# Optimization experiments

Measured on AMD Instinct MI355X. Metric: run time of the kernel, lower is better.

Reference implementation:

```python
import jax, jax.numpy as jnp
from jax import lax
import numpy as np

B, C, H, W = 4, 1024, 64, 64
HEAD_DIM = 8
HEADS = C // HEAD_DIM  # 128
EPS = 1e-15
BN_EPS = 1e-5
DN = ('NCHW', 'OIHW', 'NCHW')


def setup_inputs() -> dict:
    key = jax.random.key(0)
    ks = jax.random.split(key, 8)
    s = lambda k, shp, scale: jax.random.normal(k, shp, jnp.float32) * scale
    return {
        'x': s(ks[0], (B, C, H, W), 1.0),
        'Wq': s(ks[1], (C, C), C ** -0.5),
        'Wk': s(ks[2], (C, C), C ** -0.5),
        'Wv': s(ks[3], (C, C), C ** -0.5),
        'dw_w': s(ks[4], (3 * C, 1, 5, 5), 0.2),          # depthwise, groups=3C
        'pw_w': s(ks[5], (3 * C, HEAD_DIM, 1, 1), 0.3),   # 1x1 grouped, groups=3*heads
        'Wout': s(ks[6], (C, 2 * C), (2 * C) ** -0.5),
        'gamma': jnp.ones((C,), jnp.float32),
        'beta': jnp.zeros((C,), jnp.float32),
    }


def _forward(x, Wq, Wk, Wv, dw_w, pw_w, Wout, gamma, beta):
    b, c, h, w = x.shape
    n = h * w
    hbhwc = jnp.moveaxis(x, 1, -1)                      # B H W C
    q = hbhwc @ Wq.T
    k = hbhwc @ Wk.T
    v = hbhwc @ Wv.T
    qkv = jnp.moveaxis(jnp.concatenate([q, k, v], -1), -1, 1)  # B 3C H W
    # multiscale branch: depthwise kxk then grouped 1x1
    ms = lax.conv_general_dilated(qkv, dw_w, (1, 1), 'SAME',
                                  feature_group_count=3 * c, dimension_numbers=DN)
    ms = lax.conv_general_dilated(ms, pw_w, (1, 1), 'VALID',
                                  feature_group_count=3 * HEADS, dimension_numbers=DN)
    hs = jnp.concatenate([qkv, ms], axis=1)             # B 6C H W
    hs = hs.astype(jnp.float32).reshape(b, -1, 3 * HEAD_DIM, n)  # B ht 3d N
    q, k, v = jnp.split(hs, 3, axis=2)                  # each B ht d N
    q = jax.nn.relu(q)
    k = jax.nn.relu(k)
    v = jnp.pad(v, ((0, 0), (0, 0), (0, 1), (0, 0)), constant_values=1.0)  # B ht d+1 N
    scores = jnp.einsum('bhdn,bhen->bhde', v, k)        # B ht d+1 d
    out = jnp.einsum('bhde,bhen->bhdn', scores, q)      # B ht d+1 N
    out = out[:, :, :-1] / (out[:, :, -1:] + EPS)       # B ht d N
    out = out.reshape(b, -1, h, w)                      # B 2C H W
    out = jnp.moveaxis(jnp.moveaxis(out, 1, -1) @ Wout.T, -1, 1)  # B C H W
    # batch norm (batch statistics, affine)
    mean = out.mean(axis=(0, 2, 3), keepdims=True)
    var = out.var(axis=(0, 2, 3), keepdims=True)
    gb = lambda p: p[None, :, None, None]
    return (out - mean) * lax.rsqrt(var + BN_EPS) * gb(gamma) + gb(beta)


def reference(x, Wq, Wk, Wv, dw_w, pw_w, Wout, gamma, beta):
    return _forward(x, Wq, Wk, Wv, dw_w, pw_w, Wout, gamma, beta)
```

## Files before the change

kernel.cpp:

```cpp
#include <hip/hip_runtime.h>


typedef short bf16x8 __attribute__((ext_vector_type(8)));
typedef float f32x4 __attribute__((ext_vector_type(4)));

__device__ __forceinline__ float bf2f(unsigned short u) {
  union { unsigned int i; float f; } w; w.i = ((unsigned int)u) << 16; return w.f;
}
__device__ __forceinline__ unsigned short f2bf(float f) {
  union { float f; unsigned int i; } w; w.f = f;
  return (unsigned short)((w.i + 0x7fffu + ((w.i >> 16) & 1u)) >> 16);
}

__device__ __forceinline__ void gload16(const void* g, void* l) {
  __builtin_amdgcn_global_load_lds(
      (const __attribute__((address_space(1))) void*)g,
      (__attribute__((address_space(3))) void*)l, 16, 0, 0);
}

static constexpr int BB = 4, CC = 1024, NN = 4096;
static constexpr int C3 = 3 * CC;
static constexpr int C2 = 2 * CC;
static constexpr int MROWS = BB * NN;

__global__ __launch_bounds__(256) void k_transpose_both(const float* __restrict__ x,
                                                        float* __restrict__ xTf,
                                                        unsigned short* __restrict__ xTb) {
  __shared__ float tile[32][33];
  const int c0 = blockIdx.y << 5, n0 = blockIdx.x << 5;
  const int tx = threadIdx.x & 31, ty = threadIdx.x >> 5;
#pragma unroll
  for (int i = 0; i < 32; i += 8)
    tile[ty + i][tx] = x[((size_t)(c0 + ty + i)) * NN + n0 + tx];
  __syncthreads();
#pragma unroll
  for (int i = 0; i < 32; i += 8) {
    const float v = tile[tx][ty + i];
    const size_t idx = ((size_t)(n0 + ty + i)) * CC + c0 + tx;
    xTf[idx] = v;
    xTb[idx] = f2bf(v);
  }
}

__global__ void k_cvt(const float* __restrict__ src, unsigned short* __restrict__ dst, int n4) {
  int i = blockIdx.x * 256 + threadIdx.x;
  if (i < n4) {
    float4 v = ((const float4*)src)[i];
    ushort4 o;
    o.x = f2bf(v.x); o.y = f2bf(v.y); o.z = f2bf(v.z); o.w = f2bf(v.w);
    ((ushort4*)dst)[i] = o;
  }
}

__global__ __launch_bounds__(256) void k_wpack(const float* __restrict__ Wq,
                                               const float* __restrict__ Wk,
                                               const float* __restrict__ Wv,
                                               float* __restrict__ Wpack) {
  const int j = blockIdx.x;
  const int c = 24 * (j >> 3) + (j & 7);
  const float* src = (c < CC) ? (Wq + (size_t)c * CC)
                   : (c < 2 * CC) ? (Wk + (size_t)(c - CC) * CC)
                   : (Wv + (size_t)(c - 2 * CC) * CC);
  const int t = threadIdx.x;
  ((float4*)(Wpack + (size_t)j * CC))[t] = ((const float4*)src)[t];
}

__global__ __launch_bounds__(256) void gemm_bt(const unsigned short* __restrict__ A,
                                               const unsigned short* __restrict__ Bmat,
                                               float* __restrict__ Cout,
                                               int M, int N, int K) {
  __shared__ __align__(16) unsigned short lA[128 * 32];
  __shared__ __align__(16) unsigned short lB[128 * 32];
  const int bx = blockIdx.x, by = blockIdx.y;
  const int tid = threadIdx.x, lane = tid & 63, wid = tid >> 6;
  const int wm = wid >> 1, wn = wid & 1;

  const int srow = wid * 32 + (lane >> 2);
  const int skoff = (lane & 3) * 8;
  const unsigned short* Ag = A + (size_t)(bx * 128 + srow) * K + skoff;
  const unsigned short* Bg = Bmat + (size_t)(by * 128 + srow) * K + skoff;
  unsigned short* lAw = &lA[(wid * 32) * 32];
  unsigned short* lBw = &lB[(wid * 32) * 32];

  f32x4 acc[4][4] = {};

  for (int kt = 0; kt < K; kt += 32) {
    gload16(Ag + kt, lAw);
    gload16(Ag + kt + (size_t)16 * K, lAw + 16 * 32);
    gload16(Bg + kt, lBw);
    gload16(Bg + kt + (size_t)16 * K, lBw + 16 * 32);
    __syncthreads();

    const int fr = lane & 15, fkk = (lane >> 4) * 8;
    bf16x8 af[4], bfr[4];
#pragma unroll
    for (int i = 0; i < 4; ++i) {
      af[i]  = *reinterpret_cast<const bf16x8*>(&lA[(wm * 64 + i * 16 + fr) * 32 + fkk]);
      bfr[i] = *reinterpret_cast<const bf16x8*>(&lB[(wn * 64 + i * 16 + fr) * 32 + fkk]);
    }
#pragma unroll
    for (int i = 0; i < 4; ++i)
#pragma unroll
      for (int j = 0; j < 4; ++j)
        acc[i][j] = __builtin_amdgcn_mfma_f32_16x16x32_bf16(af[i], bfr[j], acc[i][j], 0, 0, 0);
    __syncthreads();
  }

  const int fr = lane & 15, fg = lane >> 4;
#pragma unroll
  for (int i = 0; i < 4; ++i) {
    const int row0 = bx * 128 + wm * 64 + i * 16 + fg * 4;
#pragma unroll
    for (int j = 0; j < 4; ++j) {
      const int col = by * 128 + wn * 64 + j * 16 + fr;
#pragma unroll
      for (int r = 0; r < 4; ++r)
        Cout[(size_t)(row0 + r) * N + col] = acc[i][j][r];
    }
  }
}

__global__ __launch_bounds__(256) void k_qnp(const float* __restrict__ xTf,
                                             const float* __restrict__ Wpack,
                                             float* __restrict__ qkvT) {
  __shared__ float lA[16][68];
  __shared__ float lB[16][68];
  const int bm = blockIdx.x * 64, bj = blockIdx.y * 64;
  const int t = threadIdx.x;
  const int lane = t & 63, wid = t >> 6;
  const int tj = t & 15, tm = t >> 4;

  float acc[4][4] = {{0.f}};

  for (int k0 = 0; k0 < CC; k0 += 16) {
    const float4 av = *(const float4*)(xTf + (size_t)(bm + lane) * CC + k0 + wid * 4);
    const float4 bv = *(const float4*)(Wpack + (size_t)(bj + lane) * CC + k0 + wid * 4);
    __syncthreads();
    lA[wid * 4 + 0][lane] = av.x; lA[wid * 4 + 1][lane] = av.y;
    lA[wid * 4 + 2][lane] = av.z; lA[wid * 4 + 3][lane] = av.w;
    lB[wid * 4 + 0][lane] = bv.x; lB[wid * 4 + 1][lane] = bv.y;
    lB[wid * 4 + 2][lane] = bv.z; lB[wid * 4 + 3][lane] = bv.w;
    __syncthreads();
#pragma unroll
    for (int kk = 0; kk < 16; ++kk) {
      const float4 a = *(const float4*)&lA[kk][tm * 4];
      const float4 b = *(const float4*)&lB[kk][tj * 4];
      const float af[4] = {a.x, a.y, a.z, a.w};
      const float bf[4] = {b.x, b.y, b.z, b.w};
#pragma unroll
      for (int i = 0; i < 4; ++i)
#pragma unroll
        for (int j = 0; j < 4; ++j)
          acc[i][j] = fmaf(af[i], bf[j], acc[i][j]);
    }
  }

#pragma unroll
  for (int i = 0; i < 4; ++i) {
    const int row = bm + tm * 4 + i;
#pragma unroll
    for (int j = 0; j < 4; ++j) {
      const int jj = bj + tj * 4 + j;
      const int c = 24 * (jj >> 3) + (jj & 7);
      qkvT[(size_t)row * C3 + c] = acc[i][j];
    }
  }
}

__global__ __launch_bounds__(256) void k_conv_ms(const float* __restrict__ qkvT,
                                                 const float* __restrict__ dw_w,
                                                 const float* __restrict__ pw_w,
                                                 float* __restrict__ msT) {
  __shared__ __align__(16) float tin[20][20][8];
  __shared__ float wdw[8][25];
  __shared__ float wpw[8][8];
  const int g = blockIdx.y;
  const int ty0 = (blockIdx.x >> 2) << 4, tx0 = (blockIdx.x & 3) << 4;
  const int tid = threadIdx.x;

  if (tid < 200) wdw[tid / 25][tid % 25] = dw_w[(size_t)(g * 8 + tid / 25) * 25 + tid % 25];
  if (tid < 64) wpw[tid >> 3][tid & 7] = pw_w[(size_t)(g * 8 + (tid >> 3)) * 8 + (tid & 7)];

  for (int p = tid; p < 400; p += 256) {
    const int iy = p / 20, ix = p % 20;
    const int gy = ty0 + iy - 2, gx = tx0 + ix - 2;
    float4 a = make_float4(0, 0, 0, 0), b4 = a;
    if (gy >= 0 && gy < 64 && gx >= 0 && gx < 64) {
      const float* s = &qkvT[((size_t)(gy * 64 + gx)) * C3 + g * 8];
      a = *(const float4*)s;
      b4 = *(const float4*)(s + 4);
    }
    *(float4*)&tin[iy][ix][0] = a;
    *(float4*)&tin[iy][ix][4] = b4;
  }
  __syncthreads();

  const int ty = tid >> 4, tx = tid & 15;
  double acc[8] = {0, 0, 0, 0, 0, 0, 0, 0};
#pragma unroll
  for (int dy = 0; dy < 5; ++dy)
#pragma unroll
    for (int dx = 0; dx < 5; ++dx) {
#pragma unroll
      for (int ci = 0; ci < 8; ++ci)
        acc[ci] += (double)wdw[ci][dy * 5 + dx] * (double)tin[ty + dy][tx + dx][ci];
    }
  float o[8];
#pragma unroll
  for (int co = 0; co < 8; ++co) {
    double s = 0.0;
#pragma unroll
    for (int ci = 0; ci < 8; ++ci) s += (double)wpw[co][ci] * acc[ci];
    o[co] = (float)s;
  }
  const int n = (ty0 + ty) * 64 + tx0 + tx;
  float* d = &msT[((size_t)n) * C3 + g * 8];
  *(float4*)d = make_float4(o[0], o[1], o[2], o[3]);
  *(float4*)(d + 4) = make_float4(o[4], o[5], o[6], o[7]);
}

__global__ __launch_bounds__(256) void k_attn(const float* __restrict__ qkvT,
                                              const float* __restrict__ msT,
                                              unsigned short* __restrict__ attn) {
  const int h = blockIdx.x;
  const float* src = (h < 128) ? qkvT + h * 24 : msT + (h - 128) * 24;
  const int tid = threadIdx.x, lane = tid & 63, wid = tid >> 6;

  float s[72];
#pragma unroll
  for (int i = 0; i < 72; ++i) s[i] = 0.f;

  for (int n = tid; n < NN; n += 256) {
    const float* p = src + (size_t)n * C3;
    float4 k0 = *(const float4*)(p + 8), k1 = *(const float4*)(p + 12);
    float4 v0 = *(const float4*)(p + 16), v1 = *(const float4*)(p + 20);
    float kf[8] = {fmaxf(k0.x, 0.f), fmaxf(k0.y, 0.f), fmaxf(k0.z, 0.f), fmaxf(k0.w, 0.f),
                   fmaxf(k1.x, 0.f), fmaxf(k1.y, 0.f), fmaxf(k1.z, 0.f), fmaxf(k1.w, 0.f)};
    float vf[8] = {v0.x, v0.y, v0.z, v0.w, v1.x, v1.y, v1.z, v1.w};
#pragma unroll
    for (int d = 0; d < 8; ++d)
#pragma unroll
      for (int e = 0; e < 8; ++e) s[d * 8 + e] += vf[d] * kf[e];
#pragma unroll
    for (int e = 0; e < 8; ++e) s[64 + e] += kf[e];
  }

  __shared__ float red[4][72];
  __shared__ float sc[72];
#pragma unroll
  for (int i = 0; i < 72; ++i) {
    float v = s[i];
#pragma unroll
    for (int off = 32; off > 0; off >>= 1) v += __shfl_xor(v, off, 64);
    if (lane == 0) red[wid][i] = v;
  }
  __syncthreads();
  if (tid < 72) sc[tid] = red[0][tid] + red[1][tid] + red[2][tid] + red[3][tid];
  __syncthreads();

  float sl[72];
#pragma unroll
  for (int i = 0; i < 72; ++i) sl[i] = sc[i];

  for (int n = tid; n < NN; n += 256) {
    const float* p = src + (size_t)n * C3;
    float4 q0 = *(const float4*)p, q1 = *(const float4*)(p + 4);
    float qf[8] = {fmaxf(q0.x, 0.f), fmaxf(q0.y, 0.f), fmaxf(q0.z, 0.f), fmaxf(q0.w, 0.f),
                   fmaxf(q1.x, 0.f), fmaxf(q1.y, 0.f), fmaxf(q1.z, 0.f), fmaxf(q1.w, 0.f)};
    float o[9];
#pragma unroll
    for (int d = 0; d < 9; ++d) {
      float t = 0.f;
#pragma unroll
      for (int e = 0; e < 8; ++e) t += sl[d * 8 + e] * qf[e];
      o[d] = t;
    }
    const float inv = 1.f / (o[8] + 1e-15f);
    union { unsigned short u[8]; uint4 v; } res;
#pragma unroll
    for (int d = 0; d < 8; ++d) res.u[d] = f2bf(o[d] * inv);
    *(uint4*)&attn[((size_t)n) * C2 + h * 8] = res.v;
  }
}

__global__ __launch_bounds__(256) void k_bn_stats(const float* __restrict__ out2,
                                                  float* __restrict__ part) {
  const int ch = blockIdx.x * 256 + threadIdx.x;
  const int r0 = blockIdx.y << 8;
  float s = 0.f, s2 = 0.f;
  for (int i = 0; i < 256; ++i) {
    float v = out2[(size_t)(r0 + i) * CC + ch];
    s += v; s2 += v * v;
  }
  part[((size_t)blockIdx.y * 2 + 0) * CC + ch] = s;
  part[((size_t)blockIdx.y * 2 + 1) * CC + ch] = s2;
}

__global__ __launch_bounds__(256) void k_bn_reduce(const float* __restrict__ part,
                                                   float* __restrict__ stats) {
  const int ch = blockIdx.x * 256 + threadIdx.x;
  float s = 0.f, s2 = 0.f;
  for (int i = 0; i < 64; ++i) {
    s += part[((size_t)i * 2 + 0) * CC + ch];
    s2 += part[((size_t)i * 2 + 1) * CC + ch];
  }
  stats[ch] = s;
  stats[CC + ch] = s2;
}

__global__ __launch_bounds__(256) void k_bn_apply(const float* __restrict__ out2,
                                                  const float* __restrict__ stats,
                                                  const float* __restrict__ gamma,
                                                  const float* __restrict__ beta,
                                                  float* __restrict__ out) {
  __shared__ float tile[32][33];
  const int b = blockIdx.z;
  const int c0 = blockIdx.y << 5, n0 = blockIdx.x << 5;
  const int tx = threadIdx.x & 31, ty = threadIdx.x >> 5;
  const int c = c0 + tx;
  const float mean = stats[c] * (1.f / 16384.f);
  const float var = stats[CC + c] * (1.f / 16384.f) - mean * mean;
  const float scale = gamma[c] * rsqrtf(var + 1e-5f);
  const float shift = beta[c] - mean * scale;
#pragma unroll
  for (int i = 0; i < 32; i += 8)
    tile[ty + i][tx] = out2[((size_t)b * NN + n0 + ty + i) * CC + c] * scale + shift;
  __syncthreads();
#pragma unroll
  for (int i = 0; i < 32; i += 8)
    out[((size_t)b * CC + c0 + ty + i) * NN + n0 + tx] = tile[tx][ty + i];
}

extern "C" void kernel_launch(void* const* d_in, const int* in_sizes, int n_in,
                              void* d_out, int out_size, void* d_ws, size_t ws_size,
                              hipStream_t stream) {
  const float* x     = (const float*)d_in[0];
  const float* Wq    = (const float*)d_in[1];
  const float* Wk    = (const float*)d_in[2];
  const float* Wv    = (const float*)d_in[3];
  const float* dw_w  = (const float*)d_in[4];
  const float* pw_w  = (const float*)d_in[5];
  const float* Wout  = (const float*)d_in[6];
  const float* gamma = (const float*)d_in[7];
  const float* beta  = (const float*)d_in[8];
  float* out = (float*)d_out;
  (void)ws_size; (void)in_sizes; (void)n_in; (void)out_size;

  char* ws = (char*)d_ws;
  const size_t MB = 1024 * 1024;
  float*          qkvT = (float*)(ws + 0);
  float*          msT  = (float*)(ws + 48 * MB);
  float*          xTf  = (float*)(ws + 96 * MB);
  unsigned short* xTb  = (unsigned short*)(ws + 112 * MB);
  unsigned short* Wqkv = (unsigned short*)(ws + 120 * MB);
  float*          Wpack= (float*)(ws + 126 * MB);
  unsigned short* WoutB= (unsigned short*)(ws + 130 * MB);
  float*          part = (float*)(ws + 134 * MB);
  float*          stats= (float*)(ws + 135 * MB);
  float*          out2 = (float*)(ws + 0);
  unsigned short* attnB= (unsigned short*)d_out;

  k_cvt<<<dim3(CC * CC / 4 / 256), 256, 0, stream>>>(Wq, Wqkv, CC * CC / 4);
  k_cvt<<<dim3(CC * CC / 4 / 256), 256, 0, stream>>>(Wk, Wqkv + (size_t)CC * CC, CC * CC / 4);
  k_cvt<<<dim3(CC * CC / 4 / 256), 256, 0, stream>>>(Wv, Wqkv + (size_t)2 * CC * CC, CC * CC / 4);
  k_wpack<<<dim3(CC), 256, 0, stream>>>(Wq, Wk, Wv, Wpack);
  k_cvt<<<dim3(CC * C2 / 4 / 256), 256, 0, stream>>>(Wout, WoutB, CC * C2 / 4);

  for (int b = 0; b < BB; ++b) {
    k_transpose_both<<<dim3(NN / 32, CC / 32), 256, 0, stream>>>(x + (size_t)b * CC * NN, xTf, xTb);
    gemm_bt<<<dim3(NN / 128, C3 / 128), 256, 0, stream>>>(xTb, Wqkv, qkvT, NN, C3, CC);
    k_qnp<<<dim3(NN / 64, CC / 64), 256, 0, stream>>>(xTf, Wpack, qkvT);
    k_conv_ms<<<dim3(16, C3 / 8), 256, 0, stream>>>(qkvT, dw_w, pw_w, msT);
    k_attn<<<dim3(256), 256, 0, stream>>>(qkvT, msT, attnB + (size_t)b * NN * C2);
  }

  gemm_bt<<<dim3(MROWS / 128, CC / 128), 256, 0, stream>>>(attnB, WoutB, out2, MROWS, CC, C2);

  k_bn_stats<<<dim3(CC / 256, 64), 256, 0, stream>>>(out2, part);
  k_bn_reduce<<<dim3(CC / 256), 256, 0, stream>>>(part, stats);
  k_bn_apply<<<dim3(NN / 32, CC / 32, BB), 256, 0, stream>>>(out2, stats, gamma, beta, out);
}
```

Before: 1.447 ms.

## Skip redundant q-channel bf16 GEMM and enlarge fp32 q GEMM tiles

The bf16 MFMA QKV GEMM used to compute all 3C output channels, and the fp32 k_qnp kernel then overwrote the q-type channels. A new packed weight (k and v rows only) and a dedicated gemm_kv now compute just the 2C channels that are kept, writing them straight to their interleaved positions. The fp32 q GEMM also moves to 128x128 tiles with 512 threads and two accumulator blocks per thread, for more reuse from shared memory. This removes a third of the MFMA GEMM work, but the larger fp32 tile raises register pressure, which may lower occupancy.

```diff
diff --git a/kernel.cpp b/kernel.cpp
--- a/kernel.cpp
+++ b/kernel.cpp
@@ -65,6 +65,78 @@
   ((float4*)(Wpack + (size_t)j * CC))[t] = ((const float4*)src)[t];
 }
 
+__global__ __launch_bounds__(256) void k_wkv(const float* __restrict__ Wq,
+                                             const float* __restrict__ Wk,
+                                             const float* __restrict__ Wv,
+                                             unsigned short* __restrict__ Wkv) {
+  const int jj = blockIdx.x;
+  const int c = 24 * (jj >> 4) + 8 + (jj & 15);
+  const float* src = (c < CC) ? (Wq + (size_t)c * CC)
+                   : (c < 2 * CC) ? (Wk + (size_t)(c - CC) * CC)
+                   : (Wv + (size_t)(c - 2 * CC) * CC);
+  const int t = threadIdx.x;
+  float4 v = ((const float4*)src)[t];
+  ushort4 o;
+  o.x = f2bf(v.x); o.y = f2bf(v.y); o.z = f2bf(v.z); o.w = f2bf(v.w);
+  ((ushort4*)(Wkv + (size_t)jj * CC))[t] = o;
+}
+
+__global__ __launch_bounds__(256) void gemm_kv(const unsigned short* __restrict__ A,
+                                               const unsigned short* __restrict__ Bmat,
+                                               float* __restrict__ qkvT) {
+  __shared__ __align__(16) unsigned short lA[128 * 32];
+  __shared__ __align__(16) unsigned short lB[128 * 32];
+  const int bx = blockIdx.x, by = blockIdx.y;
+  const int tid = threadIdx.x, lane = tid & 63, wid = tid >> 6;
+  const int wm = wid >> 1, wn = wid & 1;
+  const int K = CC;
+
+  const int srow = wid * 32 + (lane >> 2);
+  const int skoff = (lane & 3) * 8;
+  const unsigned short* Ag = A + (size_t)(bx * 128 + srow) * K + skoff;
+  const unsigned short* Bg = Bmat + (size_t)(by * 128 + srow) * K + skoff;
+  unsigned short* lAw = &lA[(wid * 32) * 32];
+  unsigned short* lBw = &lB[(wid * 32) * 32];
+
+  f32x4 acc[4][4] = {};
+
+  for (int kt = 0; kt < K; kt += 32) {
+    gload16(Ag + kt, lAw);
+    gload16(Ag + kt + (size_t)16 * K, lAw + 16 * 32);
+    gload16(Bg + kt, lBw);
+    gload16(Bg + kt + (size_t)16 * K, lBw + 16 * 32);
+    __syncthreads();
+
+    const int fr = lane & 15, fkk = (lane >> 4) * 8;
+    bf16x8 af[4], bfr[4];
+#pragma unroll
+    for (int i = 0; i < 4; ++i) {
+      af[i]  = *reinterpret_cast<const bf16x8*>(&lA[(wm * 64 + i * 16 + fr) * 32 + fkk]);
+      bfr[i] = *reinterpret_cast<const bf16x8*>(&lB[(wn * 64 + i * 16 + fr) * 32 + fkk]);
+    }
+#pragma unroll
+    for (int i = 0; i < 4; ++i)
+#pragma unroll
+      for (int j = 0; j < 4; ++j)
+        acc[i][j] = __builtin_amdgcn_mfma_f32_16x16x32_bf16(af[i], bfr[j], acc[i][j], 0, 0, 0);
+    __syncthreads();
+  }
+
+  const int fr = lane & 15, fg = lane >> 4;
+#pragma unroll
+  for (int i = 0; i < 4; ++i) {
+    const int row0 = bx * 128 + wm * 64 + i * 16 + fg * 4;
+#pragma unroll
+    for (int j = 0; j < 4; ++j) {
+      const int jj = by * 128 + wn * 64 + j * 16 + fr;
+      const int c = 24 * (jj >> 4) + 8 + (jj & 15);
+#pragma unroll
+      for (int r = 0; r < 4; ++r)
+        qkvT[(size_t)(row0 + r) * C3 + c] = acc[i][j][r];
+    }
+  }
+}
+
 __global__ __launch_bounds__(256) void gemm_bt(const unsigned short* __restrict__ A,
                                                const unsigned short* __restrict__ Bmat,
                                                float* __restrict__ Cout,
@@ -120,38 +192,47 @@
   }
 }
 
-__global__ __launch_bounds__(256) void k_qnp(const float* __restrict__ xTf,
+__global__ __launch_bounds__(512) void k_qnp(const float* __restrict__ xTf,
                                              const float* __restrict__ Wpack,
                                              float* __restrict__ qkvT) {
-  __shared__ float lA[16][68];
-  __shared__ float lB[16][68];
-  const int bm = blockIdx.x * 64, bj = blockIdx.y * 64;
+  __shared__ float lA[16][132];
+  __shared__ float lB[16][132];
+  const int bm = blockIdx.x * 128, bj = blockIdx.y * 128;
   const int t = threadIdx.x;
-  const int lane = t & 63, wid = t >> 6;
+  const int mat = t >> 8;
+  const int rr = (t & 255) >> 1;
+  const int hh = t & 1;
+  const float* gsrc = mat ? (Wpack + (size_t)(bj + rr) * CC + hh * 8)
+                          : (xTf  + (size_t)(bm + rr) * CC + hh * 8);
   const int tj = t & 15, tm = t >> 4;
 
-  float acc[4][4] = {{0.f}};
+  float acc[2][4][4] = {};
 
   for (int k0 = 0; k0 < CC; k0 += 16) {
-    const float4 av = *(const float4*)(xTf + (size_t)(bm + lane) * CC + k0 + wid * 4);
-    const float4 bv = *(const float4*)(Wpack + (size_t)(bj + lane) * CC + k0 + wid * 4);
-    __syncthreads();
-    lA[wid * 4 + 0][lane] = av.x; lA[wid * 4 + 1][lane] = av.y;
-    lA[wid * 4 + 2][lane] = av.z; lA[wid * 4 + 3][lane] = av.w;
-    lB[wid * 4 + 0][lane] = bv.x; lB[wid * 4 + 1][lane] = bv.y;
-    lB[wid * 4 + 2][lane] = bv.z; lB[wid * 4 + 3][lane] = bv.w;
+    const float4 g0 = *(const float4*)(gsrc + k0);
+    const float4 g1 = *(const float4*)(gsrc + k0 + 4);
+    __syncthreads();
+    float (*dst)[132] = mat ? lB : lA;
+    dst[hh * 8 + 0][rr] = g0.x; dst[hh * 8 + 1][rr] = g0.y;
+    dst[hh * 8 + 2][rr] = g0.z; dst[hh * 8 + 3][rr] = g0.w;
+    dst[hh * 8 + 4][rr] = g1.x; dst[hh * 8 + 5][rr] = g1.y;
+    dst[hh * 8 + 6][rr] = g1.z; dst[hh * 8 + 7][rr] = g1.w;
     __syncthreads();
 #pragma unroll
     for (int kk = 0; kk < 16; ++kk) {
-      const float4 a = *(const float4*)&lA[kk][tm * 4];
-      const float4 b = *(const float4*)&lB[kk][tj * 4];
-      const float af[4] = {a.x, a.y, a.z, a.w};
-      const float bf[4] = {b.x, b.y, b.z, b.w};
+      const float4 av  = *(const float4*)&lA[kk][tm * 4];
+      const float4 bv0 = *(const float4*)&lB[kk][tj * 4];
+      const float4 bv1 = *(const float4*)&lB[kk][64 + tj * 4];
+      const float af[4]  = {av.x, av.y, av.z, av.w};
+      const float bf0[4] = {bv0.x, bv0.y, bv0.z, bv0.w};
+      const float bf1[4] = {bv1.x, bv1.y, bv1.z, bv1.w};
 #pragma unroll
       for (int i = 0; i < 4; ++i)
 #pragma unroll
-        for (int j = 0; j < 4; ++j)
-          acc[i][j] = fmaf(af[i], bf[j], acc[i][j]);
+        for (int j = 0; j < 4; ++j) {
+          acc[0][i][j] = fmaf(af[i], bf0[j], acc[0][i][j]);
+          acc[1][i][j] = fmaf(af[i], bf1[j], acc[1][i][j]);
+        }
     }
   }
 
@@ -159,11 +240,13 @@
   for (int i = 0; i < 4; ++i) {
     const int row = bm + tm * 4 + i;
 #pragma unroll
-    for (int j = 0; j < 4; ++j) {
-      const int jj = bj + tj * 4 + j;
-      const int c = 24 * (jj >> 3) + (jj & 7);
-      qkvT[(size_t)row * C3 + c] = acc[i][j];
-    }
+    for (int jb = 0; jb < 2; ++jb)
+#pragma unroll
+      for (int j = 0; j < 4; ++j) {
+        const int jj = bj + jb * 64 + tj * 4 + j;
+        const int c = 24 * (jj >> 3) + (jj & 7);
+        qkvT[(size_t)row * C3 + c] = acc[jb][i][j];
+      }
   }
 }
 
@@ -352,7 +435,7 @@
   float*          msT  = (float*)(ws + 48 * MB);
   float*          xTf  = (float*)(ws + 96 * MB);
   unsigned short* xTb  = (unsigned short*)(ws + 112 * MB);
-  unsigned short* Wqkv = (unsigned short*)(ws + 120 * MB);
+  unsigned short* Wkv  = (unsigned short*)(ws + 120 * MB);
   float*          Wpack= (float*)(ws + 126 * MB);
   unsigned short* WoutB= (unsigned short*)(ws + 130 * MB);
   float*          part = (float*)(ws + 134 * MB);
@@ -360,16 +443,14 @@
   float*          out2 = (float*)(ws + 0);
   unsigned short* attnB= (unsigned short*)d_out;
 
-  k_cvt<<<dim3(CC * CC / 4 / 256), 256, 0, stream>>>(Wq, Wqkv, CC * CC / 4);
-  k_cvt<<<dim3(CC * CC / 4 / 256), 256, 0, stream>>>(Wk, Wqkv + (size_t)CC * CC, CC * CC / 4);
-  k_cvt<<<dim3(CC * CC / 4 / 256), 256, 0, stream>>>(Wv, Wqkv + (size_t)2 * CC * CC, CC * CC / 4);
+  k_wkv<<<dim3(C2), 256, 0, stream>>>(Wq, Wk, Wv, Wkv);
   k_wpack<<<dim3(CC), 256, 0, stream>>>(Wq, Wk, Wv, Wpack);
   k_cvt<<<dim3(CC * C2 / 4 / 256), 256, 0, stream>>>(Wout, WoutB, CC * C2 / 4);
 
   for (int b = 0; b < BB; ++b) {
     k_transpose_both<<<dim3(NN / 32, CC / 32), 256, 0, stream>>>(x + (size_t)b * CC * NN, xTf, xTb);
-    gemm_bt<<<dim3(NN / 128, C3 / 128), 256, 0, stream>>>(xTb, Wqkv, qkvT, NN, C3, CC);
-    k_qnp<<<dim3(NN / 64, CC / 64), 256, 0, stream>>>(xTf, Wpack, qkvT);
+    gemm_kv<<<dim3(NN / 128, C2 / 128), 256, 0, stream>>>(xTb, Wkv, qkvT);
+    k_qnp<<<dim3(NN / 128, CC / 128), 512, 0, stream>>>(xTf, Wpack, qkvT);
     k_conv_ms<<<dim3(16, C3 / 8), 256, 0, stream>>>(qkvT, dw_w, pw_w, msT);
     k_attn<<<dim3(256), 256, 0, stream>>>(qkvT, msT, attnB + (size_t)b * NN * C2);
   }
```

Result: faster. 1.385 ms (-4.3%).
